# Optimization experiments

Hardware: AMD Instinct MI355X
Metric: run time of the kernel (lower is better)

The kernel has to match this reference:

```python
import jax, jax.numpy as jnp
import numpy as np

B = 512        # graphs per batch
N_NODES = 64   # nodes per graph
IN_CH = 256
EMBED = 64
TOPK = 20
NEG_SLOPE = 0.2


def setup_inputs() -> dict:
    key = jax.random.key(0)
    ks = jax.random.split(key, 6)
    N = B * N_NODES
    x = jax.random.normal(ks[0], (N, IN_CH), dtype=jnp.float32)
    # fully-connected graph WITH self loops, per graph, sorted source-major
    src = jnp.repeat(jnp.arange(N_NODES, dtype=jnp.int32), N_NODES)  # [n*n]
    dst = jnp.tile(jnp.arange(N_NODES, dtype=jnp.int32), N_NODES)    # [n*n]
    offs = (jnp.arange(B, dtype=jnp.int32) * N_NODES)[:, None]       # [B,1]
    l = (src[None, :] + offs).reshape(-1)
    r = (dst[None, :] + offs).reshape(-1)
    edge_index = jnp.stack([l, r]).astype(jnp.int32)                 # [2, B*n*n]
    batch = jnp.repeat(jnp.arange(B, dtype=jnp.int32), N_NODES)      # [N]
    glorot = lambda k, sh: jax.random.uniform(k, sh, jnp.float32,
                                              -1.0, 1.0) * np.sqrt(6.0 / (sh[0] + sh[-1]))
    Wl = glorot(ks[1], (EMBED, IN_CH))
    bl = jnp.zeros((EMBED,), jnp.float32)
    Wr = glorot(ks[2], (EMBED, IN_CH))
    br = jnp.zeros((EMBED,), jnp.float32)
    att = glorot(ks[3], (1, EMBED))
    return {"x": x, "edge_index": edge_index, "batch": batch,
            "Wl": Wl, "bl": bl, "Wr": Wr, "br": br, "att": att}


def reference(x, edge_index, batch, Wl, bl, Wr, br, att):
    N = x.shape[0]
    x_l = x @ Wl.T + bl                      # [N, D]
    x_r = x @ Wr.T + br                      # [N, D]
    l, r = edge_index[0], edge_index[1]
    # edge gather + GAT-style score
    e = jax.nn.leaky_relu(x_l[l] + x_r[r], negative_slope=NEG_SLOPE)  # [E, D]
    alpha = (e * att[0]).sum(axis=-1)                                  # [E]
    # segment softmax grouped by source node l (each group is non-empty)
    m = jax.ops.segment_max(alpha, l, num_segments=N)
    a = jnp.exp(alpha - m[l])
    s = jax.ops.segment_sum(a, l, num_segments=N)
    a = a / s[l]
    # kNN sparsify: zero the diagonal then per-row topk
    a3 = a.reshape(B, N_NODES, N_NODES)
    a3 = a3 * (1.0 - jnp.eye(N_NODES, dtype=a3.dtype))
    attention, indices = jax.lax.top_k(a3, TOPK)     # [B, n, k] sorted desc
    attention = attention.reshape(-1)                 # [B*n*k]
    offs = (jnp.arange(B, dtype=jnp.int32) * N_NODES)[:, None]
    index_i = (jnp.repeat(jnp.arange(N_NODES, dtype=jnp.int32), TOPK)[None, :]
               + offs).reshape(-1)
    index_j = (indices.astype(jnp.int32)
               + (jnp.arange(B, dtype=jnp.int32) * N_NODES)[:, None, None]).reshape(-1)
    new_edge_index = jnp.stack([index_i, index_j])    # [2, B*n*k]
    return new_edge_index, attention
```

## Files before the change

### kernel.cpp

```cpp
#include <hip/hip_runtime.h>
#include <stdint.h>

#define NGRAPH 512
#define NN 64
#define INCH 256
#define TOPK 20
#define EPR 655360

typedef __attribute__((ext_vector_type(8))) short bf16x8;
typedef __attribute__((ext_vector_type(4))) float f32x4;

#define XLF   0
#define XRF   4352
#define ALF   8704
#define LISTS 0
#define MROW  13056
#define SROW  13568
#define SLOF  14080
#define SROF  14144
#define ATTO  14208
#define SMEM_DW 14272

static __device__ __forceinline__ uint32_t f2bfbits(float f) {
  uint32_t u = __float_as_uint(f);
  return (u + 0x7FFFu + ((u >> 16) & 1u)) >> 16;
}
static __device__ __forceinline__ uint32_t pk2(float a, float b) {
  return f2bfbits(a) | (f2bfbits(b) << 16);
}

__global__ __launch_bounds__(256) void wpack(const float* __restrict__ Wl,
                                             const float* __restrict__ Wr,
                                             uint32_t* __restrict__ ws) {
  const int t = blockIdx.x * 256 + threadIdx.x;
  const float* src = (t < 8192) ? Wl : Wr;
  const int p = t & 8191;
  float2 v = *(const float2*)(src + (size_t)p * 2);
  ws[t] = pk2(v.x, v.y);
}

__global__ __launch_bounds__(512, 4) void gat_fused(
    const float* __restrict__ x,
    const uint32_t* __restrict__ ws,
    const float* __restrict__ blv,
    const float* __restrict__ brv,
    const float* __restrict__ att,
    float* __restrict__ out)
{
  __shared__ __align__(16) uint32_t smemU[SMEM_DW];
  float* smemF = (float*)smemU;

  const int b    = blockIdx.x;
  const int t    = threadIdx.x;
  const int w    = t >> 6;
  const int lane = t & 63;
  const int quad = lane >> 4;
  const int lo   = lane & 15;
  const int nodeBase = b * NN;

  if (t < 64) smemF[ATTO + t] = att[t];

  const int half = w >> 2;
  const int r0   = (w & 3) * 16;
  f32x4 acc[4];
  #pragma unroll
  for (int ct = 0; ct < 4; ++ct) acc[ct] = (f32x4){0.f, 0.f, 0.f, 0.f};

  const uint4* wsV = (const uint4*)ws;
  #pragma unroll
  for (int ks = 0; ks < 8; ++ks) {
    const int k0 = ks * 32 + quad * 8;
    const float* ap = x + (size_t)(nodeBase + r0 + lo) * INCH + k0;
    float4 a0 = *(const float4*)ap;
    float4 a1 = *(const float4*)(ap + 4);
    uint4 au = { pk2(a0.x, a0.y), pk2(a0.z, a0.w), pk2(a1.x, a1.y), pk2(a1.z, a1.w) };
    bf16x8 afrag = __builtin_bit_cast(bf16x8, au);
    #pragma unroll
    for (int ct = 0; ct < 4; ++ct) {
      const int n = ct * 16 + lo;
      uint4 bu = wsV[half * 2048 + n * 32 + ks * 4 + quad];
      bf16x8 bfrag = __builtin_bit_cast(bf16x8, bu);
      acc[ct] = __builtin_amdgcn_mfma_f32_16x16x32_bf16(afrag, bfrag, acc[ct], 0, 0, 0);
    }
  }

  {
    const int dstBase = half ? XRF : XLF;
    const float* bias = half ? brv : blv;
    #pragma unroll
    for (int ct = 0; ct < 4; ++ct) {
      const int c = ct * 16 + lo;
      const float bb = bias[c];
      f32x4 v = { acc[ct][0] + bb, acc[ct][1] + bb, acc[ct][2] + bb, acc[ct][3] + bb };
      *(f32x4*)&smemF[dstBase + c * 68 + r0 + quad * 4] = v;
    }
  }
  __syncthreads();

  if (t < 128) {
    const int i = t & 63;
    const int base = (t < 64) ? XLF : XRF;
    float s = 0.f;
    #pragma unroll 8
    for (int d = 0; d < 64; ++d)
      s = fmaf(smemF[ATTO + d], smemF[base + d * 68 + i], s);
    smemF[((t < 64) ? SLOF : SROF) + i] = s;
  }
  __syncthreads();

  const int i0 = (t >> 4) * 2;
  const int j0 = (t & 15) * 4;
  float pacc[2][4];
  #pragma unroll
  for (int a = 0; a < 2; ++a)
    #pragma unroll
    for (int c = 0; c < 4; ++c) pacc[a][c] = 0.f;

  #pragma unroll 4
  for (int d = 0; d < 64; ++d) {
    float xl0 = smemF[XLF + d * 68 + i0];
    float xl1 = smemF[XLF + d * 68 + i0 + 1];
    f32x4 xr  = *(const f32x4*)&smemF[XRF + d * 68 + j0];
    const float ad = smemF[ATTO + d];
    #pragma unroll
    for (int c = 0; c < 4; ++c) {
      float s0 = xl0 + xr[c];
      float s1 = xl1 + xr[c];
      pacc[0][c] = fmaf(ad, fabsf(s0), pacc[0][c]);
      pacc[1][c] = fmaf(ad, fabsf(s1), pacc[1][c]);
    }
  }
  {
    f32x4 srv = *(const f32x4*)&smemF[SROF + j0];
    #pragma unroll
    for (int a = 0; a < 2; ++a) {
      const float sl = smemF[SLOF + i0 + a];
      f32x4 v;
      #pragma unroll
      for (int c = 0; c < 4; ++c)
        v[c] = 0.6f * (sl + srv[c]) + 0.4f * pacc[a][c];
      *(f32x4*)&smemF[ALF + (i0 + a) * 68 + j0] = v;
    }
  }
  __syncthreads();

  {
    const int row = t & 63;
    const int seg = t >> 6;
    const int cb  = seg * 8;
    f32x4 f0 = *(const f32x4*)&smemF[ALF + row * 68 + cb];
    f32x4 f1 = *(const f32x4*)&smemF[ALF + row * 68 + cb + 4];
    float fr[8] = { f0[0], f0[1], f0[2], f0[3], f1[0], f1[1], f1[2], f1[3] };

    float mp = fr[0];
    #pragma unroll
    for (int e = 1; e < 8; ++e) mp = fmaxf(mp, fr[e]);
    float sp = 0.f;
    #pragma unroll
    for (int e = 0; e < 8; ++e) sp += __expf(fr[e] - mp);

    uint32_t tk[8];
    #pragma unroll
    for (int k = 0; k < 8; ++k) tk[k] = 0u;
    #pragma unroll
    for (int e = 0; e < 8; ++e) {
      const int j = cb + e;
      uint32_t u = __float_as_uint(fr[e]);
      uint32_t key = u ^ ((uint32_t)((int32_t)u >> 31) | 0x80000000u);
      key = (key & 0xFFFFFFC0u) | (uint32_t)(63 - j);
      key = (j == row) ? 0u : key;
      #pragma unroll
      for (int k = 7; k >= 1; --k)
        tk[k] = (key > tk[k]) ? ((key < tk[k - 1]) ? key : tk[k - 1]) : tk[k];
      tk[0] = (key > tk[0]) ? key : tk[0];
    }
    #pragma unroll
    for (int k = 0; k < 8; ++k)
      smemU[LISTS + row * 65 + cb + k] = tk[k];
    smemF[MROW + seg * 64 + row] = mp;
    smemF[SROW + seg * 64 + row] = sp;
  }
  __syncthreads();

  if (t < 64) {
    const int row = t;
    const int lb = LISTS + row * 65;
    float m = smemF[MROW + row];
    #pragma unroll
    for (int p = 1; p < 8; ++p) m = fmaxf(m, smemF[MROW + p * 64 + row]);
    float S = 0.f;
    #pragma unroll
    for (int p = 0; p < 8; ++p)
      S += smemF[SROW + p * 64 + row] * __expf(smemF[MROW + p * 64 + row] - m);
    const float invS = 1.0f / S;

    uint32_t h0 = smemU[lb + 0],  h1 = smemU[lb + 8],  h2 = smemU[lb + 16], h3 = smemU[lb + 24];
    uint32_t h4 = smemU[lb + 32], h5 = smemU[lb + 40], h6 = smemU[lb + 48], h7 = smemU[lb + 56];
    int p0 = 0, p1 = 0, p2 = 0, p3 = 0, p4 = 0, p5 = 0, p6 = 0, p7 = 0;
    float va[TOPK], vj[TOPK];

    #pragma unroll
    for (int k = 0; k < TOPK; ++k) {
      uint32_t m01 = (h0 > h1) ? h0 : h1;
      uint32_t m23 = (h2 > h3) ? h2 : h3;
      uint32_t m45 = (h4 > h5) ? h4 : h5;
      uint32_t m67 = (h6 > h7) ? h6 : h7;
      uint32_t ma = (m01 > m23) ? m01 : m23;
      uint32_t mb = (m45 > m67) ? m45 : m67;
      uint32_t key = (ma > mb) ? ma : mb;
      const int wsel = (key == h0) ? 0 : (key == h1) ? 1 : (key == h2) ? 2 :
                       (key == h3) ? 3 : (key == h4) ? 4 : (key == h5) ? 5 :
                       (key == h6) ? 6 : 7;

      uint32_t ub = (key & 0x80000000u) ? (key ^ 0x80000000u) : ~key;
      float alpha = __uint_as_float(ub & 0xFFFFFFC0u);
      const int j = 63 - (int)(key & 63u);
      va[k] = __expf(alpha - m) * invS;
      vj[k] = (float)(nodeBase + j);

      int np = ((wsel == 0) ? p0 : (wsel == 1) ? p1 : (wsel == 2) ? p2 : (wsel == 3) ? p3 :
                (wsel == 4) ? p4 : (wsel == 5) ? p5 : (wsel == 6) ? p6 : p7) + 1;
      uint32_t hn = (np < 8) ? smemU[lb + wsel * 8 + np] : 0u;
      p0 += (wsel == 0); p1 += (wsel == 1); p2 += (wsel == 2); p3 += (wsel == 3);
      p4 += (wsel == 4); p5 += (wsel == 5); p6 += (wsel == 6); p7 += (wsel == 7);
      h0 = (wsel == 0) ? hn : h0;  h1 = (wsel == 1) ? hn : h1;
      h2 = (wsel == 2) ? hn : h2;  h3 = (wsel == 3) ? hn : h3;
      h4 = (wsel == 4) ? hn : h4;  h5 = (wsel == 5) ? hn : h5;
      h6 = (wsel == 6) ? hn : h6;  h7 = (wsel == 7) ? hn : h7;
    }

    const int g = nodeBase + row;
    const float vi = (float)g;
    float4* o0 = (float4*)(out + (size_t)g * 20);
    float4* o1 = (float4*)(out + EPR + (size_t)g * 20);
    float4* o2 = (float4*)(out + 2 * (size_t)EPR + (size_t)g * 20);
    const float4 vi4 = { vi, vi, vi, vi };
    #pragma unroll
    for (int kk = 0; kk < 5; ++kk) {
      o0[kk] = vi4;
      o1[kk] = (float4){ vj[4 * kk], vj[4 * kk + 1], vj[4 * kk + 2], vj[4 * kk + 3] };
      o2[kk] = (float4){ va[4 * kk], va[4 * kk + 1], va[4 * kk + 2], va[4 * kk + 3] };
    }
  }
}

extern "C" void kernel_launch(void* const* d_in, const int* in_sizes, int n_in,
                              void* d_out, int out_size, void* d_ws, size_t ws_size,
                              hipStream_t stream) {
  const float* x   = (const float*)d_in[0];
  const float* Wl  = (const float*)d_in[3];
  const float* bl  = (const float*)d_in[4];
  const float* Wr  = (const float*)d_in[5];
  const float* br  = (const float*)d_in[6];
  const float* att = (const float*)d_in[7];
  uint32_t* wsW = (uint32_t*)d_ws;

  wpack<<<dim3(64), dim3(256), 0, stream>>>(Wl, Wr, wsW);
  gat_fused<<<dim3(NGRAPH), dim3(512), 0, stream>>>(x, wsW, bl, br, att, (float*)d_out);
}
```

Before: 129.7 us.

## Split fused GAT kernel into projection and score/topk kernels via workspace

```diff
diff --git a/kernel.cpp b/kernel.cpp
--- a/kernel.cpp
+++ b/kernel.cpp
@@ -7,19 +7,14 @@
 #define TOPK 20
 #define EPR 655360
 
+#define XLR_U32 0
+#define SL_F32  2097152
+#define SR_F32  2129920
+#define WPK_U32 2162688
+
 typedef __attribute__((ext_vector_type(8))) short bf16x8;
 typedef __attribute__((ext_vector_type(4))) float f32x4;
-
-#define XLF   0
-#define XRF   4352
-#define ALF   8704
-#define LISTS 0
-#define MROW  13056
-#define SROW  13568
-#define SLOF  14080
-#define SROF  14144
-#define ATTO  14208
-#define SMEM_DW 14272
+typedef __attribute__((ext_vector_type(2))) float f32x2;
 
 static __device__ __forceinline__ uint32_t f2bfbits(float f) {
   uint32_t u = __float_as_uint(f);
@@ -28,27 +23,26 @@
 static __device__ __forceinline__ uint32_t pk2(float a, float b) {
   return f2bfbits(a) | (f2bfbits(b) << 16);
 }
+static __device__ __forceinline__ float lo16f(uint32_t p) { return __uint_as_float(p << 16); }
+static __device__ __forceinline__ float hi16f(uint32_t p) { return __uint_as_float(p & 0xFFFF0000u); }
 
 __global__ __launch_bounds__(256) void wpack(const float* __restrict__ Wl,
                                              const float* __restrict__ Wr,
-                                             uint32_t* __restrict__ ws) {
+                                             uint32_t* __restrict__ wsU) {
   const int t = blockIdx.x * 256 + threadIdx.x;
   const float* src = (t < 8192) ? Wl : Wr;
   const int p = t & 8191;
   float2 v = *(const float2*)(src + (size_t)p * 2);
-  ws[t] = pk2(v.x, v.y);
-}
-
-__global__ __launch_bounds__(512, 4) void gat_fused(
-    const float* __restrict__ x,
-    const uint32_t* __restrict__ ws,
-    const float* __restrict__ blv,
-    const float* __restrict__ brv,
-    const float* __restrict__ att,
-    float* __restrict__ out)
-{
-  __shared__ __align__(16) uint32_t smemU[SMEM_DW];
-  float* smemF = (float*)smemU;
+  wsU[WPK_U32 + t] = pk2(v.x, v.y);
+}
+
+__global__ __launch_bounds__(256) void k1(const float* __restrict__ x,
+                                          uint32_t* __restrict__ wsU,
+                                          const float* __restrict__ blv,
+                                          const float* __restrict__ brv,
+                                          const float* __restrict__ att) {
+  __shared__ __align__(16) float lds[128 * 68];
+  float* wsF = (float*)wsU;
 
   const int b    = blockIdx.x;
   const int t    = threadIdx.x;
@@ -56,85 +50,140 @@
   const int lane = t & 63;
   const int quad = lane >> 4;
   const int lo   = lane & 15;
-  const int nodeBase = b * NN;
-
-  if (t < 64) smemF[ATTO + t] = att[t];
-
-  const int half = w >> 2;
-  const int r0   = (w & 3) * 16;
-  f32x4 acc[4];
+
+  f32x4 acc[8];
   #pragma unroll
-  for (int ct = 0; ct < 4; ++ct) acc[ct] = (f32x4){0.f, 0.f, 0.f, 0.f};
-
-  const uint4* wsV = (const uint4*)ws;
+  for (int ct = 0; ct < 8; ++ct) acc[ct] = (f32x4){0.f, 0.f, 0.f, 0.f};
+  const int r0 = w * 16;
+  const uint4* wpk = (const uint4*)(wsU + WPK_U32);
+
   #pragma unroll
   for (int ks = 0; ks < 8; ++ks) {
     const int k0 = ks * 32 + quad * 8;
-    const float* ap = x + (size_t)(nodeBase + r0 + lo) * INCH + k0;
+    const float* ap = x + (size_t)(b * NN + r0 + lo) * INCH + k0;
     float4 a0 = *(const float4*)ap;
     float4 a1 = *(const float4*)(ap + 4);
     uint4 au = { pk2(a0.x, a0.y), pk2(a0.z, a0.w), pk2(a1.x, a1.y), pk2(a1.z, a1.w) };
     bf16x8 afrag = __builtin_bit_cast(bf16x8, au);
     #pragma unroll
-    for (int ct = 0; ct < 4; ++ct) {
-      const int n = ct * 16 + lo;
-      uint4 bu = wsV[half * 2048 + n * 32 + ks * 4 + quad];
+    for (int ct = 0; ct < 8; ++ct) {
+      const int nfull = (ct & 3) * 16 + lo + ((ct >= 4) ? 64 : 0);
+      uint4 bu = wpk[nfull * 32 + ks * 4 + quad];
       bf16x8 bfrag = __builtin_bit_cast(bf16x8, bu);
       acc[ct] = __builtin_amdgcn_mfma_f32_16x16x32_bf16(afrag, bfrag, acc[ct], 0, 0, 0);
     }
   }
 
-  {
-    const int dstBase = half ? XRF : XLF;
-    const float* bias = half ? brv : blv;
-    #pragma unroll
-    for (int ct = 0; ct < 4; ++ct) {
-      const int c = ct * 16 + lo;
-      const float bb = bias[c];
-      f32x4 v = { acc[ct][0] + bb, acc[ct][1] + bb, acc[ct][2] + bb, acc[ct][3] + bb };
-      *(f32x4*)&smemF[dstBase + c * 68 + r0 + quad * 4] = v;
-    }
+  #pragma unroll
+  for (int ct = 0; ct < 8; ++ct) {
+    const int d = (ct & 3) * 16 + lo;
+    const int drow = d + ((ct < 4) ? 0 : 64);
+    const float bias = ((ct < 4) ? blv : brv)[d];
+    float* dst = &lds[drow * 68 + r0 + quad * 4];
+    *(f32x2*)(dst)     = (f32x2){ acc[ct][0] + bias, acc[ct][1] + bias };
+    *(f32x2*)(dst + 2) = (f32x2){ acc[ct][2] + bias, acc[ct][3] + bias };
   }
   __syncthreads();
 
   if (t < 128) {
     const int i = t & 63;
-    const int base = (t < 64) ? XLF : XRF;
+    const int dbase = (t < 64) ? 0 : 64;
     float s = 0.f;
     #pragma unroll 8
     for (int d = 0; d < 64; ++d)
-      s = fmaf(smemF[ATTO + d], smemF[base + d * 68 + i], s);
-    smemF[((t < 64) ? SLOF : SROF) + i] = s;
+      s = fmaf(att[d], lds[(dbase + d) * 68 + i], s);
+    wsF[((t < 64) ? SL_F32 : SR_F32) + b * NN + i] = s;
+  }
+
+  {
+    const int drow = t >> 1;
+    const int off  = (t & 1) * 32;
+    const float* src = &lds[drow * 68 + off];
+    uint4 o[4];
+    #pragma unroll
+    for (int q = 0; q < 4; ++q) {
+      float4 f0 = *(const float4*)(src + q * 8);
+      float4 f1 = *(const float4*)(src + q * 8 + 4);
+      o[q] = (uint4){ pk2(f0.x, f0.y), pk2(f0.z, f0.w), pk2(f1.x, f1.y), pk2(f1.z, f1.w) };
+    }
+    uint4* dst = (uint4*)(wsU + XLR_U32 + b * 4096 + drow * 32 + (t & 1) * 16);
+    #pragma unroll
+    for (int q = 0; q < 4; ++q) dst[q] = o[q];
+  }
+}
+
+#define XLT   0
+#define XRT   2304
+#define ALF   6656
+#define LISTS 0
+#define MROW  8832
+#define SROW  9088
+#define SLL   9344
+#define SRL   9376
+#define ATTL  9440
+#define SMEM_DW 9504
+
+__global__ __launch_bounds__(256) void k2(const uint32_t* __restrict__ wsU,
+                                          const float* __restrict__ att,
+                                          float* __restrict__ out) {
+  __shared__ __align__(16) uint32_t smemU[SMEM_DW];
+  float* smemF = (float*)smemU;
+  const float* wsF = (const float*)wsU;
+
+  const int bx = blockIdx.x;
+  const int g  = bx >> 1;
+  const int h  = bx & 1;
+  const int t  = threadIdx.x;
+  const int nodeBase = g * NN;
+
+  {
+    const int c = t & 15;
+    #pragma unroll
+    for (int k = 0; k < 4; ++k) {
+      const int d = (t >> 4) + 16 * k;
+      uint32_t u = wsU[XLR_U32 + g * 4096 + d * 32 + h * 16 + c];
+      *(f32x2*)&smemF[XLT + d * 36 + 2 * c] = (f32x2){ lo16f(u), hi16f(u) };
+    }
+    const int c2 = t & 31;
+    #pragma unroll
+    for (int k = 0; k < 8; ++k) {
+      const int d = (t >> 5) + 8 * k;
+      uint32_t u = wsU[XLR_U32 + g * 4096 + (64 + d) * 32 + c2];
+      *(f32x2*)&smemF[XRT + d * 68 + 2 * c2] = (f32x2){ lo16f(u), hi16f(u) };
+    }
+    if (t < 32)        smemF[SLL + t]       = wsF[SL_F32 + g * NN + h * 32 + t];
+    else if (t < 96)   smemF[SRL + t - 32]  = wsF[SR_F32 + g * NN + (t - 32)];
+    else if (t < 160)  smemF[ATTL + t - 96] = att[t - 96];
   }
   __syncthreads();
 
-  const int i0 = (t >> 4) * 2;
-  const int j0 = (t & 15) * 4;
-  float pacc[2][4];
-  #pragma unroll
-  for (int a = 0; a < 2; ++a)
-    #pragma unroll
-    for (int c = 0; c < 4; ++c) pacc[a][c] = 0.f;
-
-  #pragma unroll 4
-  for (int d = 0; d < 64; ++d) {
-    float xl0 = smemF[XLF + d * 68 + i0];
-    float xl1 = smemF[XLF + d * 68 + i0 + 1];
-    f32x4 xr  = *(const f32x4*)&smemF[XRF + d * 68 + j0];
-    const float ad = smemF[ATTO + d];
-    #pragma unroll
-    for (int c = 0; c < 4; ++c) {
-      float s0 = xl0 + xr[c];
-      float s1 = xl1 + xr[c];
-      pacc[0][c] = fmaf(ad, fabsf(s0), pacc[0][c]);
-      pacc[1][c] = fmaf(ad, fabsf(s1), pacc[1][c]);
-    }
-  }
-  {
-    f32x4 srv = *(const f32x4*)&smemF[SROF + j0];
-    #pragma unroll
-    for (int a = 0; a < 2; ++a) {
-      const float sl = smemF[SLOF + i0 + a];
+  if (t < 128) {
+    const int i0 = (t >> 4) * 4;
+    const int j0 = (t & 15) * 4;
+    float pacc[4][4];
+    #pragma unroll
+    for (int a = 0; a < 4; ++a)
+      #pragma unroll
+      for (int c = 0; c < 4; ++c) pacc[a][c] = 0.f;
+
+    #pragma unroll 4
+    for (int d = 0; d < 64; ++d) {
+      f32x4 xlv = *(const f32x4*)&smemF[XLT + d * 36 + i0];
+      f32x4 xrv = *(const f32x4*)&smemF[XRT + d * 68 + j0];
+      const float ad = smemF[ATTL + d];
+      #pragma unroll
+      for (int a = 0; a < 4; ++a) {
+        #pragma unroll
+        for (int c = 0; c < 4; ++c) {
+          float s = xlv[a] + xrv[c];
+          pacc[a][c] = fmaf(ad, fabsf(s), pacc[a][c]);
+        }
+      }
+    }
+    f32x4 srv = *(const f32x4*)&smemF[SRL + j0];
+    #pragma unroll
+    for (int a = 0; a < 4; ++a) {
+      const float sl = smemF[SLL + i0 + a];
       f32x4 v;
       #pragma unroll
       for (int c = 0; c < 4; ++c)
@@ -145,8 +194,8 @@
   __syncthreads();
 
   {
-    const int row = t & 63;
-    const int seg = t >> 6;
+    const int row = t & 31;
+    const int seg = t >> 5;
     const int cb  = seg * 8;
     f32x4 f0 = *(const f32x4*)&smemF[ALF + row * 68 + cb];
     f32x4 f1 = *(const f32x4*)&smemF[ALF + row * 68 + cb + 4];
@@ -159,6 +208,7 @@
     #pragma unroll
     for (int e = 0; e < 8; ++e) sp += __expf(fr[e] - mp);
 
+    const int diag = h * 32 + row;
     uint32_t tk[8];
     #pragma unroll
     for (int k = 0; k < 8; ++k) tk[k] = 0u;
@@ -168,7 +218,7 @@
       uint32_t u = __float_as_uint(fr[e]);
       uint32_t key = u ^ ((uint32_t)((int32_t)u >> 31) | 0x80000000u);
       key = (key & 0xFFFFFFC0u) | (uint32_t)(63 - j);
-      key = (j == row) ? 0u : key;
+      key = (j == diag) ? 0u : key;
       #pragma unroll
       for (int k = 7; k >= 1; --k)
         tk[k] = (key > tk[k]) ? ((key < tk[k - 1]) ? key : tk[k - 1]) : tk[k];
@@ -176,22 +226,22 @@
     }
     #pragma unroll
     for (int k = 0; k < 8; ++k)
-      smemU[LISTS + row * 65 + cb + k] = tk[k];
-    smemF[MROW + seg * 64 + row] = mp;
-    smemF[SROW + seg * 64 + row] = sp;
+      smemU[LISTS + row * 68 + cb + k] = tk[k];
+    smemF[MROW + seg * 32 + row] = mp;
+    smemF[SROW + seg * 32 + row] = sp;
   }
   __syncthreads();
 
-  if (t < 64) {
+  if (t < 32) {
     const int row = t;
-    const int lb = LISTS + row * 65;
+    const int lb = LISTS + row * 68;
     float m = smemF[MROW + row];
     #pragma unroll
-    for (int p = 1; p < 8; ++p) m = fmaxf(m, smemF[MROW + p * 64 + row]);
+    for (int p = 1; p < 8; ++p) m = fmaxf(m, smemF[MROW + p * 32 + row]);
     float S = 0.f;
     #pragma unroll
     for (int p = 0; p < 8; ++p)
-      S += smemF[SROW + p * 64 + row] * __expf(smemF[MROW + p * 64 + row] - m);
+      S += smemF[SROW + p * 32 + row] * __expf(smemF[MROW + p * 32 + row] - m);
     const float invS = 1.0f / S;
 
     uint32_t h0 = smemU[lb + 0],  h1 = smemU[lb + 8],  h2 = smemU[lb + 16], h3 = smemU[lb + 24];
@@ -212,15 +262,16 @@
                        (key == h3) ? 3 : (key == h4) ? 4 : (key == h5) ? 5 :
                        (key == h6) ? 6 : 7;
 
+      int np = ((wsel == 0) ? p0 : (wsel == 1) ? p1 : (wsel == 2) ? p2 : (wsel == 3) ? p3 :
+                (wsel == 4) ? p4 : (wsel == 5) ? p5 : (wsel == 6) ? p6 : p7) + 1;
+      uint32_t hn = (np < 8) ? smemU[lb + wsel * 8 + np] : 0u;
+
       uint32_t ub = (key & 0x80000000u) ? (key ^ 0x80000000u) : ~key;
       float alpha = __uint_as_float(ub & 0xFFFFFFC0u);
       const int j = 63 - (int)(key & 63u);
       va[k] = __expf(alpha - m) * invS;
       vj[k] = (float)(nodeBase + j);
 
-      int np = ((wsel == 0) ? p0 : (wsel == 1) ? p1 : (wsel == 2) ? p2 : (wsel == 3) ? p3 :
-                (wsel == 4) ? p4 : (wsel == 5) ? p5 : (wsel == 6) ? p6 : p7) + 1;
-      uint32_t hn = (np < 8) ? smemU[lb + wsel * 8 + np] : 0u;
       p0 += (wsel == 0); p1 += (wsel == 1); p2 += (wsel == 2); p3 += (wsel == 3);
       p4 += (wsel == 4); p5 += (wsel == 5); p6 += (wsel == 6); p7 += (wsel == 7);
       h0 = (wsel == 0) ? hn : h0;  h1 = (wsel == 1) ? hn : h1;
@@ -229,11 +280,11 @@
       h6 = (wsel == 6) ? hn : h6;  h7 = (wsel == 7) ? hn : h7;
     }
 
-    const int g = nodeBase + row;
-    const float vi = (float)g;
-    float4* o0 = (float4*)(out + (size_t)g * 20);
-    float4* o1 = (float4*)(out + EPR + (size_t)g * 20);
-    float4* o2 = (float4*)(out + 2 * (size_t)EPR + (size_t)g * 20);
+    const int gout = bx * 32 + row;
+    const float vi = (float)gout;
+    float4* o0 = (float4*)(out + (size_t)gout * 20);
+    float4* o1 = (float4*)(out + EPR + (size_t)gout * 20);
+    float4* o2 = (float4*)(out + 2 * (size_t)EPR + (size_t)gout * 20);
     const float4 vi4 = { vi, vi, vi, vi };
     #pragma unroll
     for (int kk = 0; kk < 5; ++kk) {
@@ -253,8 +304,9 @@
   const float* Wr  = (const float*)d_in[5];
   const float* br  = (const float*)d_in[6];
   const float* att = (const float*)d_in[7];
-  uint32_t* wsW = (uint32_t*)d_ws;
-
-  wpack<<<dim3(64), dim3(256), 0, stream>>>(Wl, Wr, wsW);
-  gat_fused<<<dim3(NGRAPH), dim3(512), 0, stream>>>(x, wsW, bl, br, att, (float*)d_out);
-}
+  uint32_t* wsU = (uint32_t*)d_ws;
+
+  wpack<<<dim3(64),   dim3(256), 0, stream>>>(Wl, Wr, wsU);
+  k1   <<<dim3(NGRAPH), dim3(256), 0, stream>>>(x, wsU, bl, br, att);
+  k2   <<<dim3(2 * NGRAPH), dim3(256), 0, stream>>>(wsU, att, (float*)d_out);
+}
```

After: 136.4 us. 5.1% more time.
